# Performance work log

Measured on AMD Instinct MI355X. Metric: run time of the kernel, lower is better.

## Reference

```python
import jax, jax.numpy as jnp
import numpy as np

D_MODEL = 2048
NUM_HEADS = 16
D_K = D_MODEL // NUM_HEADS
ROPE_THETA = 10000.0
B, S = 2, 2048


def setup_inputs() -> dict:
    key = jax.random.key(0)
    ks = jax.random.split(key, 5)
    std = 1.0 / np.sqrt(D_MODEL)
    return {
        "x": jax.random.normal(ks[0], (B, S, D_MODEL), jnp.float32),
        "wq": jax.random.normal(ks[1], (D_MODEL, D_MODEL), jnp.float32) * std,
        "wk": jax.random.normal(ks[2], (D_MODEL, D_MODEL), jnp.float32) * std,
        "wv": jax.random.normal(ks[3], (D_MODEL, D_MODEL), jnp.float32) * std,
        "wo": jax.random.normal(ks[4], (D_MODEL, D_MODEL), jnp.float32) * std,
        "token_positions": jnp.arange(S, dtype=jnp.int32),
    }


def _rope(x, positions):
    # x: [b, h, s, d_k]; positions: [s]
    inv_freq = 1.0 / (ROPE_THETA ** (jnp.arange(0, D_K, 2, dtype=jnp.float32) / D_K))
    freqs = positions.astype(jnp.float32)[:, None] * inv_freq[None, :]  # [s, d_k/2]
    cos, sin = jnp.cos(freqs), jnp.sin(freqs)
    x_even, x_odd = x[..., ::2], x[..., 1::2]
    out_even = x_even * cos - x_odd * sin
    out_odd = x_even * sin + x_odd * cos
    # re-interleave even/odd lanes
    return jnp.stack([out_even, out_odd], axis=-1).reshape(x.shape)


def reference(x, wq, wk, wv, wo, token_positions):
    b, s, _ = x.shape
    # projections: weight is [out, in] as in torch Linear-style einsum
    q = jnp.einsum("bsd,ed->bse", x, wq)
    k = jnp.einsum("bsd,ed->bse", x, wk)
    v = jnp.einsum("bsd,ed->bse", x, wv)
    # split heads: b s (h d) -> b h s d
    def split(t):
        return t.reshape(b, s, NUM_HEADS, D_K).transpose(0, 2, 1, 3)
    q, k, v = split(q), split(k), split(v)
    q = _rope(q, token_positions)
    k = _rope(k, token_positions)
    scores = jnp.einsum("bhmd,bhnd->bhmn", q, k) / jnp.sqrt(jnp.float32(D_K))
    causal = jnp.tril(jnp.ones((s, s), dtype=bool))
    scores = jnp.where(causal[None, None], scores, -jnp.inf)
    attn = jax.nn.softmax(scores, axis=-1)
    out = jnp.einsum("bhmn,bhnd->bhmd", attn, v)
    out = out.transpose(0, 2, 1, 3).reshape(b, s, D_MODEL)
    return jnp.einsum("em,bsm->bse", wo, out)
```

## Files before the change

kernel.cpp:

```cpp
#include <hip/hip_runtime.h>

#define S_LEN 2048
#define DM 2048
#define NH 16
#define DK 128
#define BB 2
#define BH (BB*NH)
#define GK 2048

typedef float f32x4 __attribute__((ext_vector_type(4)));
typedef __bf16 bf16x8 __attribute__((ext_vector_type(8)));
typedef __bf16 bf16x4 __attribute__((ext_vector_type(4)));
typedef unsigned int u32;

#define AS1 __attribute__((address_space(1)))
#define AS3 __attribute__((address_space(3)))

__device__ inline void gload16(const void* g, void* l){
  __builtin_amdgcn_global_load_lds((AS1 const u32*)g, (AS3 u32*)l, 16, 0, 0);
}

__device__ inline ushort f2bf(float f){
  __bf16 h = (__bf16)f;
  ushort u;
  __builtin_memcpy(&u, &h, 2);
  return u;
}

__global__ void k_conv(const float* __restrict__ x, const float* __restrict__ wq,
                       const float* __restrict__ wk, const float* __restrict__ wv,
                       const float* __restrict__ wo4,
                       ushort* __restrict__ xb, ushort* __restrict__ dqkv,
                       ushort* __restrict__ dwo,
                       const int* __restrict__ pos, float2* __restrict__ cs){
  int bid = blockIdx.x;
  if (bid >= 24576){
    int idx = (bid - 24576) * 256 + threadIdx.x;
    int s = idx >> 6, i = idx & 63;
    float inv = expf(-0.14391156831212787f * (float)i);
    float f = (float)pos[s] * inv;
    cs[idx] = make_float2(cosf(f), sinf(f));
    return;
  }
  int i = bid * 256 + threadIdx.x;
  int sel = i >> 20;
  int off = i & ((1 << 20) - 1);
  const float* s; ushort* d;
  if (sel < 2){ s = x + ((size_t)sel << 22); d = xb + ((size_t)sel << 22); }
  else if (sel == 2){ s = wq; d = dqkv; }
  else if (sel == 3){ s = wk; d = dqkv + (size_t)DM * DM; }
  else if (sel == 4){ s = wv; d = dqkv + (size_t)2 * DM * DM; }
  else { s = wo4; d = dwo; }
  float4 v = reinterpret_cast<const float4*>(s)[off];
  ushort4 o;
  o.x = f2bf(v.x); o.y = f2bf(v.y); o.z = f2bf(v.z); o.w = f2bf(v.w);
  reinterpret_cast<ushort4*>(d)[off] = o;
}

#define SBAR() do{ __builtin_amdgcn_s_barrier(); __builtin_amdgcn_sched_barrier(0); }while(0)
#define VMC(n) asm volatile("s_waitcnt vmcnt(" #n ")" ::: "memory")

#define STG(slot, srcp, tks, khh) do{ \
  const ushort* _s = (srcp) + (tks)*64 + (khh)*32; \
  gload16(_s,                    lds + (slot)*8192 + wid*512); \
  gload16(_s + (size_t)128*GK,   lds + (slot)*8192 + 4096 + wid*512); \
}while(0)

#define RD_A(slot, mh) do{ \
  af[0] = *reinterpret_cast<const bf16x8*>(ldsc + (slot)*16384 + wm*8192 + ((mh)*4+0)*1024 + frA); \
  af[1] = *reinterpret_cast<const bf16x8*>(ldsc + (slot)*16384 + wm*8192 + ((mh)*4+1)*1024 + frA); \
  af[2] = *reinterpret_cast<const bf16x8*>(ldsc + (slot)*16384 + wm*8192 + ((mh)*4+2)*1024 + frA); \
  af[3] = *reinterpret_cast<const bf16x8*>(ldsc + (slot)*16384 + wm*8192 + ((mh)*4+3)*1024 + frA); \
}while(0)

#define RD_B(slot) do{ \
  bfr[0] = *reinterpret_cast<const bf16x8*>(ldsc + (slot)*16384 + wn*4096 + 0*1024 + frA); \
  bfr[1] = *reinterpret_cast<const bf16x8*>(ldsc + (slot)*16384 + wn*4096 + 1*1024 + frA); \
  bfr[2] = *reinterpret_cast<const bf16x8*>(ldsc + (slot)*16384 + wn*4096 + 2*1024 + frA); \
  bfr[3] = *reinterpret_cast<const bf16x8*>(ldsc + (slot)*16384 + wn*4096 + 3*1024 + frA); \
}while(0)

#define MM(mh) do{ \
  __builtin_amdgcn_s_setprio(1); \
  _Pragma("unroll") \
  for (int mf2 = 0; mf2 < 4; mf2++) \
    _Pragma("unroll") \
    for (int nf = 0; nf < 4; nf++) \
      acc[(mh)*4+mf2][nf] = __builtin_amdgcn_mfma_f32_16x16x32_bf16(af[mf2], bfr[nf], acc[(mh)*4+mf2][nf], 0, 0, 0); \
  __builtin_amdgcn_s_setprio(0); \
}while(0)

__launch_bounds__(512, 2)
__global__ void k_gemm_qk(const ushort* __restrict__ A, const ushort* __restrict__ Bt,
                          const float2* __restrict__ cs,
                          ushort* __restrict__ Qh, ushort* __restrict__ Kh){
  __shared__ short lds[65536];
  const int tid = threadIdx.x, lane = tid & 63, wid = tid >> 6;
  const int wm = wid >> 2, wn = wid & 3;
  const int fr = lane & 15, fq = lane >> 4;

  const int bid = blockIdx.x;
  const int b2 = (bid & 7) * 32 + (bid >> 3);
  const int by = b2 >> 4, bx = b2 & 15;

  const int rbase = wid * 16 + (lane >> 2);
  const int kup = ((lane & 3) ^ ((lane >> 3) & 3)) * 8;
  const ushort* pa = A  + (size_t)(by * 256 + rbase) * GK + kup;
  const ushort* pb = Bt + (size_t)(bx * 256 + rbase) * GK + kup;

  const char* ldsc = (const char*)lds;
  const int frA = fr * 64 + ((fq * 16) ^ (((fr >> 1) & 3) << 4));

  f32x4 acc[8][4] = {};
  bf16x8 af[4], bfr[4];

  STG(0, pa, 0, 0); STG(1, pb, 0, 0); STG(2, pa, 0, 1); STG(3, pb, 0, 1);
  STG(4, pa, 1, 0); STG(5, pb, 1, 0);
  VMC(8);
  SBAR();

  #pragma unroll 1
  for (int it = 0; it < 16; ++it){
    const int tb  = 2 * it + 1;
    const int tn  = (2 * it + 2 < 32) ? 2 * it + 2 : 31;
    const int tn1 = (2 * it + 3 < 32) ? 2 * it + 3 : 31;
    RD_A(0, 0); RD_B(1); STG(6, pa, tb, 1);           SBAR(); MM(0); SBAR();
    RD_A(0, 1);          STG(7, pb, tb, 1);  VMC(6);  SBAR(); MM(1); SBAR();
    RD_A(2, 0); RD_B(3); STG(0, pa, tn, 0);           SBAR(); MM(0); SBAR();
    RD_A(2, 1);          STG(1, pb, tn, 0);  VMC(6);  SBAR(); MM(1); SBAR();
    RD_A(4, 0); RD_B(5); STG(2, pa, tn, 1);           SBAR(); MM(0); SBAR();
    RD_A(4, 1);          STG(3, pb, tn, 1);  VMC(6);  SBAR(); MM(1); SBAR();
    RD_A(6, 0); RD_B(7); STG(4, pa, tn1, 0);          SBAR(); MM(0); SBAR();
    RD_A(6, 1);          STG(5, pb, tn1, 0); VMC(6);  SBAR(); MM(1); SBAR();
  }

  const int rowb = by * 256 + wm * 128 + fq * 4;
  const bool isQ = (bx < 8);
  ushort* dst = isQ ? Qh : Kh;
  const float qscl = isQ ? 0.08838834764831845f : 1.0f;
  #pragma unroll
  for (int mf = 0; mf < 8; mf++)
    #pragma unroll
    for (int nf = 0; nf < 4; nf++){
      int col = bx * 256 + wn * 64 + nf * 16 + fr;
      int cg = col & 2047;
      int hh = cg >> 7, dd = cg & 127, jj = (cg >> 1) & 63;
      #pragma unroll
      for (int i = 0; i < 4; i++){
        int row = rowb + mf * 16 + i;
        int s = row & (S_LEN - 1), bb = row >> 11;
        float2 c2 = cs[s * 64 + jj];
        float v = acc[mf][nf][i];
        float p = __shfl_xor(v, 1);
        float o = (fr & 1) ? fmaf(p, c2.y, v * c2.x) : fmaf(v, c2.x, -p * c2.y);
        dst[((size_t)(bb * NH + hh) * S_LEN + s) * DK + dd] = f2bf(o * qscl);
      }
    }
}

#define WSTG_A(si, tks, khh) do{ \
  const ushort* _s = pa + (tks)*64 + (khh)*32; \
  gload16(_s,                  lds + (si)*8192 + wid*512); \
  gload16(_s + (size_t)128*GK, lds + (si)*8192 + 4096 + wid*512); \
}while(0)
#define WSTG_B(si, tks, khh) do{ \
  const ushort* _s = pb + (tks)*64 + (khh)*32; \
  gload16(_s, lds + 32768 + (si)*4096 + wid*512); \
}while(0)
#define WRD_A(si, mhf) do{ \
  af[0] = *reinterpret_cast<const bf16x8*>(ldsc + (si)*16384 + wm*4096 + ((mhf)*2+0)*1024 + frA); \
  af[1] = *reinterpret_cast<const bf16x8*>(ldsc + (si)*16384 + wm*4096 + ((mhf)*2+1)*1024 + frA); \
}while(0)
#define WRD_B(si) do{ \
  bfr[0] = *reinterpret_cast<const bf16x8*>(ldsc + 65536 + (si)*8192 + wn*4096 + 0*1024 + frA); \
  bfr[1] = *reinterpret_cast<const bf16x8*>(ldsc + 65536 + (si)*8192 + wn*4096 + 1*1024 + frA); \
  bfr[2] = *reinterpret_cast<const bf16x8*>(ldsc + 65536 + (si)*8192 + wn*4096 + 2*1024 + frA); \
  bfr[3] = *reinterpret_cast<const bf16x8*>(ldsc + 65536 + (si)*8192 + wn*4096 + 3*1024 + frA); \
}while(0)
#define WMM(mhf) do{ \
  __builtin_amdgcn_s_setprio(1); \
  _Pragma("unroll") \
  for (int k2 = 0; k2 < 2; k2++) \
    _Pragma("unroll") \
    for (int nf = 0; nf < 4; nf++) \
      acc[(mhf)*2+k2][nf] = __builtin_amdgcn_mfma_f32_16x16x32_bf16(af[k2], bfr[nf], acc[(mhf)*2+k2][nf], 0, 0, 0); \
  __builtin_amdgcn_s_setprio(0); \
}while(0)

#define WBODY() \
  WSTG_A(0, 0, 0); WSTG_B(0, 0, 0); WSTG_A(1, 0, 1); WSTG_B(1, 0, 1); \
  WSTG_A(2, 1, 0); WSTG_B(2, 1, 0); \
  VMC(6); \
  SBAR(); \
  _Pragma("unroll 1") \
  for (int it = 0; it < 16; ++it){ \
    const int tb  = 2 * it + 1; \
    const int tn  = (2 * it + 2 < 32) ? 2 * it + 2 : 31; \
    const int tn1 = (2 * it + 3 < 32) ? 2 * it + 3 : 31; \
    WRD_A(0, 0); WRD_B(0); WSTG_A(3, tb, 1);            SBAR(); WMM(0); SBAR(); \
    WRD_A(0, 1);           WSTG_B(3, tb, 1);  VMC(6);   SBAR(); WMM(1); SBAR(); \
    WRD_A(1, 0); WRD_B(1); WSTG_A(0, tn, 0);            SBAR(); WMM(0); SBAR(); \
    WRD_A(1, 1);           WSTG_B(0, tn, 0);  VMC(6);   SBAR(); WMM(1); SBAR(); \
    WRD_A(2, 0); WRD_B(2); WSTG_A(1, tn, 1);            SBAR(); WMM(0); SBAR(); \
    WRD_A(2, 1);           WSTG_B(1, tn, 1);  VMC(6);   SBAR(); WMM(1); SBAR(); \
    WRD_A(3, 0); WRD_B(3); WSTG_A(2, tn1, 0);           SBAR(); WMM(0); SBAR(); \
    WRD_A(3, 1);           WSTG_B(2, tn1, 0); VMC(6);   SBAR(); WMM(1); SBAR(); \
  }

__launch_bounds__(512, 2)
__global__ void k_gemm_v(const ushort* __restrict__ A, const ushort* __restrict__ Bt,
                         ushort* __restrict__ Vt){
  __shared__ short lds[49152];
  const int tid = threadIdx.x, lane = tid & 63, wid = tid >> 6;
  const int wm = wid >> 1, wn = wid & 1;
  const int fr = lane & 15, fq = lane >> 4;

  const int bid = blockIdx.x;
  const int b2 = (bid & 7) * 32 + (bid >> 3);
  const int by = b2 >> 4, bx = b2 & 15;

  const int rbase = wid * 16 + (lane >> 2);
  const int kup = ((lane & 3) ^ ((lane >> 3) & 3)) * 8;
  const ushort* pa = A  + (size_t)(by * 256 + rbase) * GK + kup;
  const ushort* pb = Bt + (size_t)(bx * 128 + rbase) * GK + kup;

  const char* ldsc = (const char*)lds;
  const int frA = fr * 64 + ((fq * 16) ^ (((fr >> 1) & 3) << 4));

  f32x4 acc[4][4] = {};
  bf16x8 af[2], bfr[4];

  WBODY();

  const int rowb = by * 256 + wm * 64 + fq * 4;
  #pragma unroll
  for (int mf = 0; mf < 4; mf++){
    int row0 = rowb + mf * 16;
    int s0 = row0 & (S_LEN - 1), bb = row0 >> 11;
    #pragma unroll
    for (int nf = 0; nf < 4; nf++){
      int col = bx * 128 + wn * 64 + nf * 16 + fr;
      int hh = col >> 7, dd = col & 127;
      ushort4 o;
      o.x = f2bf(acc[mf][nf][0]); o.y = f2bf(acc[mf][nf][1]);
      o.z = f2bf(acc[mf][nf][2]); o.w = f2bf(acc[mf][nf][3]);
      *reinterpret_cast<ushort4*>(&Vt[((size_t)(bb * NH + hh) * DK + dd) * S_LEN + s0]) = o;
    }
  }
}

__launch_bounds__(512, 2)
__global__ void k_gemm_wo(const ushort* __restrict__ A, const ushort* __restrict__ Bt,
                          float* __restrict__ C){
  __shared__ short lds[49152];
  const int tid = threadIdx.x, lane = tid & 63, wid = tid >> 6;
  const int wm = wid >> 1, wn = wid & 1;
  const int fr = lane & 15, fq = lane >> 4;

  const int bid = blockIdx.x;
  const int b2 = (bid & 7) * 32 + (bid >> 3);
  const int by = b2 >> 4, bx = b2 & 15;

  const int rbase = wid * 16 + (lane >> 2);
  const int kup = ((lane & 3) ^ ((lane >> 3) & 3)) * 8;
  const ushort* pa = A  + (size_t)(by * 256 + rbase) * GK + kup;
  const ushort* pb = Bt + (size_t)(bx * 128 + rbase) * GK + kup;

  const char* ldsc = (const char*)lds;
  const int frA = fr * 64 + ((fq * 16) ^ (((fr >> 1) & 3) << 4));

  f32x4 acc[4][4] = {};
  bf16x8 af[2], bfr[4];

  WBODY();

  const int orow = by * 256 + wm * 64 + fq * 4;
  const int ocol = bx * 128 + wn * 64 + fr;
  #pragma unroll
  for (int mf = 0; mf < 4; mf++)
    #pragma unroll
    for (int nf = 0; nf < 4; nf++)
      #pragma unroll
      for (int i = 0; i < 4; i++)
        C[(size_t)(orow + mf * 16 + i) * DM + ocol + nf * 16] = acc[mf][nf][i];
}

__launch_bounds__(256, 2)
__global__ void k_attn(const ushort* __restrict__ Q, const ushort* __restrict__ K,
                       const ushort* __restrict__ Vt, ushort* __restrict__ O){
  __shared__ short Kt[2][64 * 128];
  __shared__ short Vl[2][128 * 64];
  __shared__ short Pl[4][16 * 80];
  const int tid = threadIdx.x, lane = tid & 63, wid = tid >> 6;
  const int bid = blockIdx.x;
  const int pid = bid >> 5;
  const int bh = bid & 31;
  const int b = bh >> 4, h = bh & 15;
  const int fr = lane & 15, fq = lane >> 4;
  const int kswz = (fr & 6) << 5;
  const int vswz = (fr & 7) << 4;

  const ushort* kb = K  + (size_t)bh * S_LEN * DK;
  const ushort* vb = Vt + (size_t)bh * DK * S_LEN;
  char* PlB = (char*)Pl + wid * 2560;
  ushort* ob = O + (size_t)b * S_LEN * DM;

  int kro[4], kco[4], vro[4], vco[4];
  #pragma unroll
  for (int jj = 0; jj < 4; jj++){
    int ins = wid * 4 + jj;
    kro[jj] = ins * 4 + (lane >> 4);
    kco[jj] = 8 * ((lane & 15) ^ ((kro[jj] & 6) << 1));
    vro[jj] = ins * 8 + (lane >> 3);
    vco[jj] = 8 * ((lane & 7) ^ (vro[jj] & 7));
  }

  #pragma unroll 1
  for (int half = 0; half < 2; half++){
    const int j = half ? pid : 31 - pid;
    const int qr = j * 64 + wid * 16;
    const int nt = j + 1;

    bf16x8 qf[4];
    #pragma unroll
    for (int c = 0; c < 4; c++)
      qf[c] = *reinterpret_cast<const bf16x8*>(
          Q + ((size_t)bh * S_LEN + qr + fr) * DK + c * 32 + fq * 8);

    float mi = -1e30f, li = 0.f;
    f32x4 accO[8] = {};

    __syncthreads();
    {
      char* kd = (char*)Kt;
      char* vd = (char*)Vl;
      #pragma unroll
      for (int jj = 0; jj < 4; jj++){
        int ins = wid * 4 + jj;
        gload16(kb + (size_t)kro[jj] * DK + kco[jj],      kd + ins * 1024);
        gload16(vb + (size_t)vro[jj] * S_LEN + vco[jj],   vd + ins * 1024);
      }
    }
    __syncthreads();

    #pragma unroll 1
    for (int kt = 0; kt < nt; kt++){
      const int k0 = kt * 64;
      const int cur = kt & 1;
      if (kt + 1 < nt){
        const int k1 = k0 + 64;
        char* kd = (char*)Kt + (cur ^ 1) * 16384;
        char* vd = (char*)Vl + (cur ^ 1) * 16384;
        #pragma unroll
        for (int jj = 0; jj < 4; jj++){
          int ins = wid * 4 + jj;
          gload16(kb + (size_t)(k1 + kro[jj]) * DK + kco[jj],  kd + ins * 1024);
          gload16(vb + (size_t)vro[jj] * S_LEN + k1 + vco[jj], vd + ins * 1024);
        }
      }
      const char* KtB = (const char*)Kt + cur * 16384;
      const char* VlB = (const char*)Vl + cur * 16384;

      f32x4 sc[4] = {};
      #pragma unroll
      for (int c = 0; c < 4; c++){
        bf16x8 kf[4];
        #pragma unroll
        for (int ch = 0; ch < 4; ch++)
          kf[ch] = *reinterpret_cast<const bf16x8*>(
              KtB + (ch * 16 + fr) * 256 + ((c * 64 + fq * 16) ^ kswz));
        #pragma unroll
        for (int ch = 0; ch < 4; ch++)
          sc[ch] = __builtin_amdgcn_mfma_f32_16x16x32_bf16(kf[ch], qf[c], sc[ch], 0, 0, 0);
      }

      const int qrow = qr + fr;
      if (kt == nt - 1){
        #pragma unroll
        for (int ch = 0; ch < 4; ch++)
          #pragma unroll
          for (int i = 0; i < 4; i++)
            if (k0 + ch * 16 + fq * 4 + i > qrow) sc[ch][i] = -1e30f;
      }

      float mx = sc[0][0];
      #pragma unroll
      for (int ch = 0; ch < 4; ch++)
        #pragma unroll
        for (int i = 0; i < 4; i++) mx = fmaxf(mx, sc[ch][i]);
      mx = fmaxf(mx, __shfl_xor(mx, 16));
      mx = fmaxf(mx, __shfl_xor(mx, 32));

      if (!__all(mx <= mi + 8.0f)){
        float mn = fmaxf(mi, mx);
        float scl = __expf(mi - mn);
        mi = mn;
        li *= scl;
        float sclq[4];
        #pragma unroll
        for (int i = 0; i < 4; i++) sclq[i] = __shfl(scl, fq * 4 + i);
        #pragma unroll
        for (int dt = 0; dt < 8; dt++)
          #pragma unroll
          for (int i = 0; i < 4; i++) accO[dt][i] *= sclq[i];
      }

      float rs = 0.f;
      #pragma unroll
      for (int ch = 0; ch < 4; ch++)
        #pragma unroll
        for (int i = 0; i < 4; i++){
          float e = __expf(sc[ch][i] - mi);
          sc[ch][i] = e;
          rs += e;
        }
      rs += __shfl_xor(rs, 16);
      rs += __shfl_xor(rs, 32);
      li += rs;

      #pragma unroll
      for (int ch = 0; ch < 4; ch++){
        bf16x4 pk;
        pk[0] = (__bf16)sc[ch][0]; pk[1] = (__bf16)sc[ch][1];
        pk[2] = (__bf16)sc[ch][2]; pk[3] = (__bf16)sc[ch][3];
        *reinterpret_cast<bf16x4*>(PlB + fr * 160 + ch * 32 + fq * 8) = pk;
      }
      bf16x8 pf[2];
      #pragma unroll
      for (int c2 = 0; c2 < 2; c2++)
        pf[c2] = *reinterpret_cast<const bf16x8*>(PlB + fr * 160 + c2 * 64 + fq * 16);

      #pragma unroll
      for (int dt = 0; dt < 8; dt++)
        #pragma unroll
        for (int c2 = 0; c2 < 2; c2++){
          bf16x8 vf = *reinterpret_cast<const bf16x8*>(
              VlB + (dt * 16 + fr) * 128 + ((c2 * 64 + fq * 16) ^ vswz));
          accO[dt] = __builtin_amdgcn_mfma_f32_16x16x32_bf16(pf[c2], vf, accO[dt], 0, 0, 0);
        }
      __syncthreads();
    }

    float inv[4];
    #pragma unroll
    for (int i = 0; i < 4; i++) inv[i] = 1.f / __shfl(li, fq * 4 + i);
    #pragma unroll
    for (int dt = 0; dt < 8; dt++)
      #pragma unroll
      for (int i = 0; i < 4; i++){
        int row = qr + fq * 4 + i;
        ob[(size_t)row * DM + h * DK + dt * 16 + fr] = f2bf(accO[dt][i] * inv[i]);
      }
  }
}

extern "C" void kernel_launch(void* const* d_in, const int* in_sizes, int n_in,
                              void* d_out, int out_size, void* d_ws, size_t ws_size,
                              hipStream_t stream){
  const float* x  = (const float*)d_in[0];
  const float* wq = (const float*)d_in[1];
  const float* wk = (const float*)d_in[2];
  const float* wv = (const float*)d_in[3];
  const float* wo = (const float*)d_in[4];
  const int* pos  = (const int*)d_in[5];
  float* out = (float*)d_out;

  char* ws = (char*)d_ws;
  ushort* xb   = (ushort*)(ws);
  ushort* Ob   = xb;
  ushort* wqkv = (ushort*)(ws + 16777216);
  ushort* Qh   = (ushort*)(ws + 41943040);
  ushort* Kh   = (ushort*)(ws + 58720256);
  ushort* Vt   = (ushort*)(ws + 75497472);
  float2* cs   = (float2*)(ws + 92274688);
  ushort* wob  = (ushort*)(ws + 93323264);

  k_conv<<<24576 + 512, 256, 0, stream>>>(x, wq, wk, wv, wo, xb, wqkv, wob, pos, cs);

  k_gemm_qk<<<256, 512, 0, stream>>>(xb, wqkv, cs, Qh, Kh);
  k_gemm_v<<<256, 512, 0, stream>>>(xb, wqkv + (size_t)2 * DM * DM, Vt);

  k_attn<<<512, 256, 0, stream>>>(Qh, Kh, Vt, Ob);

  k_gemm_wo<<<256, 512, 0, stream>>>(Ob, wob, out);
}
```

Before: 237.6 us.

## Load K fragments directly from global memory and raise priority around MFMA blocks

Removes the double-buffered LDS staging of K tiles in the attention kernel. Each wave now loads its QK^T K fragments straight from global memory into registers, which cuts LDS usage and LDS traffic. The MFMA sections are also wrapped in s_setprio to favour matrix issue across waves. The risk is exposed global-load latency, since K is no longer prefetched a tile ahead, plus redundant K reads by all four waves (served by cache) and higher register pressure.

```diff
diff --git a/kernel.cpp b/kernel.cpp
--- a/kernel.cpp
+++ b/kernel.cpp
@@ -288,7 +288,6 @@
 __launch_bounds__(256, 2)
 __global__ void k_attn(const ushort* __restrict__ Q, const ushort* __restrict__ K,
                        const ushort* __restrict__ Vt, ushort* __restrict__ O){
-  __shared__ short Kt[2][64 * 128];
   __shared__ short Vl[2][128 * 64];
   __shared__ short Pl[4][16 * 80];
   const int tid = threadIdx.x, lane = tid & 63, wid = tid >> 6;
@@ -297,7 +296,6 @@
   const int bh = bid & 31;
   const int b = bh >> 4, h = bh & 15;
   const int fr = lane & 15, fq = lane >> 4;
-  const int kswz = (fr & 6) << 5;
   const int vswz = (fr & 7) << 4;
 
   const ushort* kb = K  + (size_t)bh * S_LEN * DK;
@@ -305,12 +303,10 @@
   char* PlB = (char*)Pl + wid * 2560;
   ushort* ob = O + (size_t)b * S_LEN * DM;
 
-  int kro[4], kco[4], vro[4], vco[4];
+  int vro[4], vco[4];
   #pragma unroll
   for (int jj = 0; jj < 4; jj++){
     int ins = wid * 4 + jj;
-    kro[jj] = ins * 4 + (lane >> 4);
-    kco[jj] = 8 * ((lane & 15) ^ ((kro[jj] & 6) << 1));
     vro[jj] = ins * 8 + (lane >> 3);
     vco[jj] = 8 * ((lane & 7) ^ (vro[jj] & 7));
   }
@@ -331,15 +327,10 @@
     f32x4 accO[8] = {};
 
     __syncthreads();
-    {
-      char* kd = (char*)Kt;
-      char* vd = (char*)Vl;
-      #pragma unroll
-      for (int jj = 0; jj < 4; jj++){
-        int ins = wid * 4 + jj;
-        gload16(kb + (size_t)kro[jj] * DK + kco[jj],      kd + ins * 1024);
-        gload16(vb + (size_t)vro[jj] * S_LEN + vco[jj],   vd + ins * 1024);
-      }
+    #pragma unroll
+    for (int jj = 0; jj < 4; jj++){
+      int ins = wid * 4 + jj;
+      gload16(vb + (size_t)vro[jj] * S_LEN + vco[jj], (char*)Vl + ins * 1024);
     }
     __syncthreads();
 
@@ -349,30 +340,31 @@
       const int cur = kt & 1;
       if (kt + 1 < nt){
         const int k1 = k0 + 64;
-        char* kd = (char*)Kt + (cur ^ 1) * 16384;
         char* vd = (char*)Vl + (cur ^ 1) * 16384;
         #pragma unroll
         for (int jj = 0; jj < 4; jj++){
           int ins = wid * 4 + jj;
-          gload16(kb + (size_t)(k1 + kro[jj]) * DK + kco[jj],  kd + ins * 1024);
           gload16(vb + (size_t)vro[jj] * S_LEN + k1 + vco[jj], vd + ins * 1024);
         }
       }
-      const char* KtB = (const char*)Kt + cur * 16384;
       const char* VlB = (const char*)Vl + cur * 16384;
 
+      bf16x8 kf[4][4];
+      #pragma unroll
+      for (int c = 0; c < 4; c++)
+        #pragma unroll
+        for (int ch = 0; ch < 4; ch++)
+          kf[c][ch] = *reinterpret_cast<const bf16x8*>(
+              kb + (size_t)(k0 + ch * 16 + fr) * DK + c * 32 + fq * 8);
+
       f32x4 sc[4] = {};
-      #pragma unroll
-      for (int c = 0; c < 4; c++){
-        bf16x8 kf[4];
+      __builtin_amdgcn_s_setprio(1);
+      #pragma unroll
+      for (int c = 0; c < 4; c++)
         #pragma unroll
         for (int ch = 0; ch < 4; ch++)
-          kf[ch] = *reinterpret_cast<const bf16x8*>(
-              KtB + (ch * 16 + fr) * 256 + ((c * 64 + fq * 16) ^ kswz));
-        #pragma unroll
-        for (int ch = 0; ch < 4; ch++)
-          sc[ch] = __builtin_amdgcn_mfma_f32_16x16x32_bf16(kf[ch], qf[c], sc[ch], 0, 0, 0);
-      }
+          sc[ch] = __builtin_amdgcn_mfma_f32_16x16x32_bf16(kf[c][ch], qf[c], sc[ch], 0, 0, 0);
+      __builtin_amdgcn_s_setprio(0);
 
       const int qrow = qr + fr;
       if (kt == nt - 1){
@@ -430,6 +422,7 @@
       for (int c2 = 0; c2 < 2; c2++)
         pf[c2] = *reinterpret_cast<const bf16x8*>(PlB + fr * 160 + c2 * 64 + fq * 16);
 
+      __builtin_amdgcn_s_setprio(1);
       #pragma unroll
       for (int dt = 0; dt < 8; dt++)
         #pragma unroll
@@ -438,6 +431,7 @@
               VlB + (dt * 16 + fr) * 128 + ((c2 * 64 + fq * 16) ^ vswz));
           accO[dt] = __builtin_amdgcn_mfma_f32_16x16x32_bf16(pf[c2], vf, accO[dt], 0, 0, 0);
         }
+      __builtin_amdgcn_s_setprio(0);
       __syncthreads();
     }
 
```

Result: slower. 302.0 us (+27.1%).
